# Kernel optimization log

Measured on AMD Instinct MI355X. Metric: run time of the kernel, lower is better.

## Reference

```python
import jax, jax.numpy as jnp
import numpy as np

NUM_EXPERTS = 8
TOP_K = 2


def setup_inputs() -> dict:
    key = jax.random.key(0)
    ks = jax.random.split(key, 8)
    B, S, D, H, E = 4, 2048, 1024, 2048, NUM_EXPERTS
    sd = 1.0 / np.sqrt(D)
    sh = 1.0 / np.sqrt(H)
    return {
        "x": jax.random.normal(ks[0], (B, S, D), dtype=jnp.float32),
        "noise": jax.random.normal(ks[1], (B, S, E), dtype=jnp.float32),
        "router_w": jax.random.normal(ks[2], (E, D), dtype=jnp.float32) * sd,
        "router_b": jnp.zeros((E,), dtype=jnp.float32),
        "noise_w": jax.random.normal(ks[3], (E, D), dtype=jnp.float32) * sd,
        "noise_b": jnp.zeros((E,), dtype=jnp.float32),
        "w1": jax.random.normal(ks[4], (E, H, D), dtype=jnp.float32) * sd,
        "w2": jax.random.normal(ks[5], (E, D, H), dtype=jnp.float32) * sh,
        "w3": jax.random.normal(ks[6], (E, H, D), dtype=jnp.float32) * sd,
    }


def reference(x, noise, router_w, router_b, noise_w, noise_b, w1, w2, w3):
    B, S, D = x.shape
    T = B * S
    xf = x.reshape(T, D)                                  # [T, D]
    noise_f = noise.reshape(T, -1)                        # [T, E]

    # Noisy top-k router
    logits = xf @ router_w.T + router_b                   # [T, E]
    noise_logits = xf @ noise_w.T + noise_b               # [T, E]
    noisy = logits + noise_f * jax.nn.softplus(noise_logits)
    top_vals, top_idx = jax.lax.top_k(noisy, TOP_K)       # [T, K]
    sparse = jnp.full_like(noisy, -jnp.inf)
    sparse = sparse.at[jnp.arange(T)[:, None], top_idx].set(top_vals)
    gates = jax.nn.softmax(sparse, axis=-1)               # [T, E]; zero off top-k

    # Expert SwiGLU combine. Gates are exactly 0 for non-selected experts, so
    # the masked gather/scatter loop of the original equals this weighted sum.
    out = jnp.zeros_like(xf)
    for i in range(NUM_EXPERTS):
        h = jax.nn.silu(xf @ w1[i].T) * (xf @ w3[i].T)    # [T, H]
        out = out + gates[:, i:i + 1] * (h @ w2[i].T)     # [T, D]
    return out.reshape(B, S, D)
```

## Files before the change

### kernel.cpp

```cpp
#include <hip/hip_runtime.h>

typedef unsigned short u16;
typedef __attribute__((ext_vector_type(8))) __bf16 bf16x8;
typedef __attribute__((ext_vector_type(8))) short short8;
typedef __attribute__((ext_vector_type(4))) float f32x4;

#define NE 8

#define SBAR()      asm volatile("s_barrier" ::: "memory")
#define WAIT_LGKM0() do { asm volatile("s_waitcnt lgkmcnt(0)" ::: "memory"); \
                          __builtin_amdgcn_sched_barrier(0); } while (0)
#define WAIT_VM4()  asm volatile("s_waitcnt vmcnt(4)" ::: "memory")
#define WAIT_VM0()  asm volatile("s_waitcnt vmcnt(0)" ::: "memory")

__device__ __forceinline__ u16 f2bf(float f) {
    union { float f; unsigned u; } v; v.f = f;
    unsigned u = v.u;
    return (u16)((u + 0x7fffu + ((u >> 16) & 1u)) >> 16);
}

__device__ __forceinline__ f32x4 mfma16(short8 a, short8 b, f32x4 c) {
    return __builtin_amdgcn_mfma_f32_16x16x32_bf16(
        __builtin_bit_cast(bf16x8, a), __builtin_bit_cast(bf16x8, b), c, 0, 0, 0);
}

__device__ __forceinline__ void gl2lds(const u16* g, u16* l) {
    __builtin_amdgcn_global_load_lds((const __attribute__((address_space(1))) void*)g,
                                     (__attribute__((address_space(3))) void*)l,
                                     16, 0, 0);
}

__global__ void cvt_kernel(const float* __restrict__ in, u16* __restrict__ out, size_t n4) {
    size_t i = (size_t)blockIdx.x * blockDim.x + threadIdx.x;
    size_t stride = (size_t)gridDim.x * blockDim.x;
    for (; i < n4; i += stride) {
        float4 v = ((const float4*)in)[i];
        ushort4 o;
        o.x = f2bf(v.x); o.y = f2bf(v.y); o.z = f2bf(v.z); o.w = f2bf(v.w);
        ((ushort4*)out)[i] = o;
    }
}

__global__ void cvt_w13_kernel(const float* __restrict__ w1, const float* __restrict__ w3,
                               u16* __restrict__ wc, int H, int D) {
    size_t n = (size_t)NE * H * (D / 4);
    size_t i = (size_t)blockIdx.x * blockDim.x + threadIdx.x;
    size_t stride = (size_t)gridDim.x * blockDim.x;
    int d4n = D / 4;
    for (; i < n; i += stride) {
        int d4 = (int)(i % d4n);
        size_t rem = i / d4n;
        int j = (int)(rem % H);
        int e = (int)(rem / H);
        float4 v1 = ((const float4*)w1)[i];
        float4 v3 = ((const float4*)w3)[i];
        ushort4 o1, o3;
        o1.x = f2bf(v1.x); o1.y = f2bf(v1.y); o1.z = f2bf(v1.z); o1.w = f2bf(v1.w);
        o3.x = f2bf(v3.x); o3.y = f2bf(v3.y); o3.z = f2bf(v3.z); o3.w = f2bf(v3.w);
        int wcrow = ((j >> 4) << 5) + (j & 15);
        size_t o = (((size_t)e * 2 * H + wcrow) * d4n + d4);
        ((ushort4*)wc)[o] = o1;
        ((ushort4*)wc)[o + (size_t)16 * d4n] = o3;
    }
}

__global__ void router_kernel(const float* __restrict__ x, const float* __restrict__ noise,
                              const float* __restrict__ rw, const float* __restrict__ rb,
                              const float* __restrict__ nw, const float* __restrict__ nb,
                              int* __restrict__ tops, float* __restrict__ gpair,
                              u16* __restrict__ xb, int T, int D) {
    int wv = threadIdx.x >> 6;
    int lane = threadIdx.x & 63;
    int t = blockIdx.x * 4 + wv;
    if (t >= T) return;

    const float4* x4 = (const float4*)(x + (size_t)t * D) + lane * 4;
    float4 xv0 = x4[0], xv1 = x4[1], xv2 = x4[2], xv3 = x4[3];

    {
        ushort4 s0, s1, s2, s3;
        s0.x = f2bf(xv0.x); s0.y = f2bf(xv0.y); s0.z = f2bf(xv0.z); s0.w = f2bf(xv0.w);
        s1.x = f2bf(xv1.x); s1.y = f2bf(xv1.y); s1.z = f2bf(xv1.z); s1.w = f2bf(xv1.w);
        s2.x = f2bf(xv2.x); s2.y = f2bf(xv2.y); s2.z = f2bf(xv2.z); s2.w = f2bf(xv2.w);
        s3.x = f2bf(xv3.x); s3.y = f2bf(xv3.y); s3.z = f2bf(xv3.z); s3.w = f2bf(xv3.w);
        ushort4* o = (ushort4*)(xb + (size_t)t * D + lane * 16);
        o[0] = s0; o[1] = s1; o[2] = s2; o[3] = s3;
    }

    float acc[2 * NE];
#pragma unroll
    for (int e = 0; e < NE; e++) {
        const float4* w4 = (const float4*)(rw + (size_t)e * D) + lane * 4;
        float4 a = w4[0], b = w4[1], c = w4[2], d = w4[3];
        acc[e] = xv0.x*a.x + xv0.y*a.y + xv0.z*a.z + xv0.w*a.w
               + xv1.x*b.x + xv1.y*b.y + xv1.z*b.z + xv1.w*b.w
               + xv2.x*c.x + xv2.y*c.y + xv2.z*c.z + xv2.w*c.w
               + xv3.x*d.x + xv3.y*d.y + xv3.z*d.z + xv3.w*d.w;
        const float4* v4 = (const float4*)(nw + (size_t)e * D) + lane * 4;
        a = v4[0]; b = v4[1]; c = v4[2]; d = v4[3];
        acc[NE + e] = xv0.x*a.x + xv0.y*a.y + xv0.z*a.z + xv0.w*a.w
                    + xv1.x*b.x + xv1.y*b.y + xv1.z*b.z + xv1.w*b.w
                    + xv2.x*c.x + xv2.y*c.y + xv2.z*c.z + xv2.w*c.w
                    + xv3.x*d.x + xv3.y*d.y + xv3.z*d.z + xv3.w*d.w;
    }
#pragma unroll
    for (int m = 1; m < 64; m <<= 1) {
#pragma unroll
        for (int k = 0; k < 2 * NE; k++) acc[k] += __shfl_xor(acc[k], m);
    }

    if (lane == 0) {
        float v0 = -1e30f, v1 = -1e30f;
        int i0 = 0, i1 = 0;
#pragma unroll
        for (int e = 0; e < NE; e++) {
            float z = acc[NE + e] + nb[e];
            float sp = (z > 20.f) ? z : log1pf(expf(z));
            float nv = acc[e] + rb[e] + noise[(size_t)t * NE + e] * sp;
            if (nv > v0) { v1 = v0; i1 = i0; v0 = nv; i0 = e; }
            else if (nv > v1) { v1 = nv; i1 = e; }
        }
        float e1 = expf(v1 - v0);
        float inv = 1.f / (1.f + e1);
        tops[t] = i0 | (i1 << 8);
        gpair[2 * t]     = inv;
        gpair[2 * t + 1] = e1 * inv;
    }
}

__global__ void build_kernel(const int* __restrict__ tops, const float* __restrict__ gpair,
                             int* __restrict__ counts, int* __restrict__ list,
                             float* __restrict__ glist, int* __restrict__ tokslot, int T) {
    int e = blockIdx.x;
    int tid = threadIdx.x, lane = tid & 63, wv = tid >> 6;
    __shared__ int wsum[4];
    __shared__ int sbase;
    if (tid == 0) sbase = 0;
    __syncthreads();
    for (int t0 = 0; t0 < T; t0 += 256) {
        int t = t0 + tid;
        int pk = tops[t];
        int i0 = pk & 0xff, i1 = (pk >> 8) & 0xff;
        bool f0 = (i0 == e), f1 = (i1 == e);
        bool f = f0 || f1;
        unsigned long long m = __ballot(f);
        int lpos = __popcll(m & (((unsigned long long)1 << lane) - 1ull));
        if (lane == 0) wsum[wv] = __popcll(m);
        __syncthreads();
        int woff = sbase;
        for (int w = 0; w < wv; w++) woff += wsum[w];
        int tot = wsum[0] + wsum[1] + wsum[2] + wsum[3];
        if (f) {
            int pos = woff + lpos;
            list[e * T + pos]  = t;
            glist[e * T + pos] = f0 ? gpair[2 * t] : gpair[2 * t + 1];
            tokslot[2 * t + (f0 ? 0 : 1)] = (e << 16) | pos;
        }
        __syncthreads();
        if (tid == 0) sbase += tot;
    }
    __syncthreads();
    if (tid == 0) counts[e] = sbase;
}

__global__ void scan_kernel(const int* __restrict__ counts, int* __restrict__ offsets,
                            int* __restrict__ bmap, int* __restrict__ nb) {
    if (threadIdx.x == 0 && blockIdx.x == 0) {
        int s = 0, t = 0;
        for (int e = 0; e < NE; e++) {
            offsets[e] = s;
            int c = counts[e];
            s += c;
            int m = (c + 255) >> 8;
            for (int i = 0; i < m; i++) bmap[t++] = (e << 16) | i;
        }
        offsets[NE] = s;
        nb[0] = t;
    }
}


#define FRAG_READS(abase, bbase, af, bf, mibase) do { \
        _Pragma("unroll") \
        for (int mi = 0; mi < 4; mi++) \
            af[mi] = *(const short8*)((abase) + aoff + ((mibase) + mi) * 512); \
        if (bf##_load) { \
            _Pragma("unroll") \
            for (int ni = 0; ni < 4; ni++) \
                bf[ni] = *(const short8*)((bbase) + boff + ni * 512); \
        } } while (0)

#define MFMA16X(af, bf, mibase) do { \
        __builtin_amdgcn_s_setprio(1); \
        _Pragma("unroll") \
        for (int mi = 0; mi < 4; mi++) \
            _Pragma("unroll") \
            for (int ni = 0; ni < 4; ni++) \
                acc[(mibase) + mi][ni] = mfma16(af[mi], bf[ni], acc[(mibase) + mi][ni]); \
        __builtin_amdgcn_s_setprio(0); } while (0)

__launch_bounds__(512, 2)
__global__ void gemm1_kernel(const u16* __restrict__ xb, const u16* __restrict__ wc,
                             const int* __restrict__ counts, const int* __restrict__ offsets,
                             const int* __restrict__ list, const float* __restrict__ glist,
                             const int* __restrict__ bmap, const int* __restrict__ nb,
                             u16* __restrict__ hb, int T, int D, int H) {
    if ((int)blockIdx.y >= nb[0]) return;
    int info = bmap[blockIdx.y];
    int e = info >> 16, mblk = info & 0xffff, nblk = blockIdx.x;
    int count = counts[e];

    __shared__ u16 sA[3 * 8192];
    __shared__ u16 sB[3 * 8192];
    __shared__ int stok[256];
    __shared__ float sgate[256];

    int tid = threadIdx.x;
    int lane = tid & 63, wid = tid >> 6;

    if (tid < 256) {
        int rr = min(mblk * 256 + tid, count - 1);
        stok[tid]  = list[e * T + rr];
        sgate[tid] = glist[e * T + rr];
    }
    __syncthreads();

    const u16* wcp = wc + ((size_t)e * 2 * H + nblk * 256) * D;

    int srow = tid >> 2, qs = tid & 3;
    int cchk = qs ^ ((srow >> 1) & 3);
    const u16* pa0 = xb + (size_t)stok[srow] * D + cchk * 8;
    const u16* pa1 = xb + (size_t)stok[128 + srow] * D + cchk * 8;
    const u16* pb0 = wcp + (size_t)srow * D + cchk * 8;
    const u16* pb1 = wcp + (size_t)(128 + srow) * D + cchk * 8;
    u16* dstA = sA + wid * 512;
    u16* dstB = sB + wid * 512;

    int r = lane & 15, q = lane >> 4;
    int cq = q ^ ((r >> 1) & 3);
    int wr = wid >> 2, wc4 = wid & 3;
    int aoff = (wr * 128 + r) * 32 + cq * 8;
    int boff = (wc4 * 64 + r) * 32 + cq * 8;

    f32x4 acc[8][4];
#pragma unroll
    for (int mi = 0; mi < 8; mi++)
#pragma unroll
        for (int ni = 0; ni < 4; ni++) acc[mi][ni] = (f32x4)0.f;

    gl2lds(pa0, dstA);          gl2lds(pb0, dstB);
    gl2lds(pa1, dstA + 4096);   gl2lds(pb1, dstB + 4096);
    pa0 += 32; pa1 += 32; pb0 += 32; pb1 += 32;
    gl2lds(pa0, dstA + 8192);          gl2lds(pb0, dstB + 8192);
    gl2lds(pa1, dstA + 8192 + 4096);   gl2lds(pb1, dstB + 8192 + 4096);
    pa0 += 32; pa1 += 32; pb0 += 32; pb1 += 32;
    WAIT_VM4();
    SBAR();

    const int nt = D >> 5;
    int cur = 0;
    for (int t = 0; t < nt; ++t) {
        const u16* abase = sA + cur * 8192;
        const u16* bbase = sB + cur * 8192;
        int stg = cur + 2; if (stg >= 3) stg -= 3;
        u16* asg = sA + stg * 8192 + wid * 512;
        u16* bsg = sB + stg * 8192 + wid * 512;
        bool st = (t + 2 < nt);

        short8 af[4], bf[4];
        const bool bf_load = true;
        FRAG_READS(abase, bbase, af, bf, 0);
        if (st) { gl2lds(pa0, asg); gl2lds(pb0, bsg); }
        SBAR();
        WAIT_LGKM0();
        MFMA16X(af, bf, 0);
        SBAR();
#pragma unroll
        for (int mi = 0; mi < 4; mi++)
            af[mi] = *(const short8*)(abase + aoff + (4 + mi) * 512);
        if (st) {
            gl2lds(pa1, asg + 4096); gl2lds(pb1, bsg + 4096);
            pa0 += 32; pa1 += 32; pb0 += 32; pb1 += 32;
        }
        SBAR();
        WAIT_LGKM0();
        MFMA16X(af, bf, 4);
        if (st) { WAIT_VM4(); } else { WAIT_VM0(); }
        SBAR();
        cur++; if (cur >= 3) cur = 0;
    }

    int hrow0 = offsets[e];
#pragma unroll
    for (int mi = 0; mi < 8; mi++) {
#pragma unroll
        for (int p = 0; p < 2; p++) {
            int col = nblk * 128 + wc4 * 32 + p * 16 + r;
#pragma unroll
            for (int tt = 0; tt < 4; tt++) {
                int lrow = wr * 128 + mi * 16 + q * 4 + tt;
                int grow = mblk * 256 + lrow;
                if (grow < count) {
                    float v = acc[mi][2 * p][tt];
                    float hv = v / (1.f + expf(-v)) * acc[mi][2 * p + 1][tt] * sgate[lrow];
                    hb[(size_t)(hrow0 + grow) * H + col] = f2bf(hv);
                }
            }
        }
    }
}

__launch_bounds__(512, 2)
__global__ void gemm2_kernel(const u16* __restrict__ hb, const u16* __restrict__ w2b,
                             const int* __restrict__ counts, const int* __restrict__ offsets,
                             const int* __restrict__ bmap, const int* __restrict__ nb,
                             float* __restrict__ o2, int T, int D, int H) {
    if ((int)blockIdx.y >= nb[0]) return;
    int info = bmap[blockIdx.y];
    int e = info >> 16, mblk = info & 0xffff, nblk = blockIdx.x;
    int count = counts[e];

    __shared__ u16 sA[3 * 8192];
    __shared__ u16 sB[3 * 8192];

    int tid = threadIdx.x;
    int lane = tid & 63, wid = tid >> 6;
    int off0 = offsets[e];
    const u16* w2p = w2b + ((size_t)e * D + nblk * 256) * H;

    int srow = tid >> 2, qs = tid & 3;
    int cchk = qs ^ ((srow >> 1) & 3);
    int ra0 = min(mblk * 256 + srow, count - 1);
    int ra1 = min(mblk * 256 + 128 + srow, count - 1);
    const u16* pa0 = hb + (size_t)(off0 + ra0) * H + cchk * 8;
    const u16* pa1 = hb + (size_t)(off0 + ra1) * H + cchk * 8;
    const u16* pb0 = w2p + (size_t)srow * H + cchk * 8;
    const u16* pb1 = w2p + (size_t)(128 + srow) * H + cchk * 8;
    u16* dstA = sA + wid * 512;
    u16* dstB = sB + wid * 512;

    int r = lane & 15, q = lane >> 4;
    int cq = q ^ ((r >> 1) & 3);
    int wr = wid >> 2, wc4 = wid & 3;
    int aoff = (wr * 128 + r) * 32 + cq * 8;
    int boff = (wc4 * 64 + r) * 32 + cq * 8;

    f32x4 acc[8][4];
#pragma unroll
    for (int mi = 0; mi < 8; mi++)
#pragma unroll
        for (int ni = 0; ni < 4; ni++) acc[mi][ni] = (f32x4)0.f;

    gl2lds(pa0, dstA);          gl2lds(pb0, dstB);
    gl2lds(pa1, dstA + 4096);   gl2lds(pb1, dstB + 4096);
    pa0 += 32; pa1 += 32; pb0 += 32; pb1 += 32;
    gl2lds(pa0, dstA + 8192);          gl2lds(pb0, dstB + 8192);
    gl2lds(pa1, dstA + 8192 + 4096);   gl2lds(pb1, dstB + 8192 + 4096);
    pa0 += 32; pa1 += 32; pb0 += 32; pb1 += 32;
    WAIT_VM4();
    SBAR();

    const int nt = H >> 5;
    int cur = 0;
    for (int t = 0; t < nt; ++t) {
        const u16* abase = sA + cur * 8192;
        const u16* bbase = sB + cur * 8192;
        int stg = cur + 2; if (stg >= 3) stg -= 3;
        u16* asg = sA + stg * 8192 + wid * 512;
        u16* bsg = sB + stg * 8192 + wid * 512;
        bool st = (t + 2 < nt);

        short8 af[4], bf[4];
        const bool bf_load = true;
        FRAG_READS(abase, bbase, af, bf, 0);
        if (st) { gl2lds(pa0, asg); gl2lds(pb0, bsg); }
        SBAR();
        WAIT_LGKM0();
        MFMA16X(af, bf, 0);
        SBAR();
#pragma unroll
        for (int mi = 0; mi < 4; mi++)
            af[mi] = *(const short8*)(abase + aoff + (4 + mi) * 512);
        if (st) {
            gl2lds(pa1, asg + 4096); gl2lds(pb1, bsg + 4096);
            pa0 += 32; pa1 += 32; pb0 += 32; pb1 += 32;
        }
        SBAR();
        WAIT_LGKM0();
        MFMA16X(af, bf, 4);
        if (st) { WAIT_VM4(); } else { WAIT_VM0(); }
        SBAR();
        cur++; if (cur >= 3) cur = 0;
    }

#pragma unroll
    for (int mi = 0; mi < 8; mi++) {
#pragma unroll
        for (int tt = 0; tt < 4; tt++) {
            int grow = mblk * 256 + wr * 128 + mi * 16 + q * 4 + tt;
            if (grow < count) {
#pragma unroll
                for (int ni = 0; ni < 4; ni++) {
                    int col = nblk * 256 + wc4 * 64 + ni * 16 + r;
                    o2[(size_t)(off0 + grow) * D + col] = acc[mi][ni][tt];
                }
            }
        }
    }
}

__global__ void combine_kernel(const float* __restrict__ o2, const int* __restrict__ tokslot,
                               const int* __restrict__ offsets, float* __restrict__ out, int D) {
    int t = blockIdx.x;
    int s0 = tokslot[2 * t], s1 = tokslot[2 * t + 1];
    size_t r0 = offsets[s0 >> 16] + (s0 & 0xffff);
    size_t r1 = offsets[s1 >> 16] + (s1 & 0xffff);
    int c = threadIdx.x * 4;
    float4 a = *(const float4*)(o2 + r0 * D + c);
    float4 b = *(const float4*)(o2 + r1 * D + c);
    float4 o; o.x = a.x + b.x; o.y = a.y + b.y; o.z = a.z + b.z; o.w = a.w + b.w;
    *(float4*)(out + (size_t)t * D + c) = o;
}

extern "C" void kernel_launch(void* const* d_in, const int* in_sizes, int n_in,
                              void* d_out, int out_size, void* d_ws, size_t ws_size,
                              hipStream_t stream) {
    const float* x     = (const float*)d_in[0];
    const float* noise = (const float*)d_in[1];
    const float* rw    = (const float*)d_in[2];
    const float* rb    = (const float*)d_in[3];
    const float* nw    = (const float*)d_in[4];
    const float* nb_   = (const float*)d_in[5];
    const float* w1    = (const float*)d_in[6];
    const float* w2    = (const float*)d_in[7];
    const float* w3    = (const float*)d_in[8];
    float* out = (float*)d_out;

    const int E = NE;
    const int D = in_sizes[2] / E;
    const int T = in_sizes[0] / D;
    const int H = in_sizes[6] / (E * D);

    auto al = [](size_t v) { return (v + 255) & ~(size_t)255; };
    char* p = (char*)d_ws;
    size_t o_counts  = 0;
    size_t o_offsets = 64;
    size_t o_nb      = 128;
    size_t o_bmap    = 256;
    size_t o_tslot   = al(o_bmap  + 2048);
    size_t o_list    = al(o_tslot + (size_t)2 * T * 4);
    size_t o_glist   = al(o_list  + (size_t)E * T * 4);
    size_t o_xb      = al(o_glist + (size_t)E * T * 4);
    size_t o_wc      = al(o_xb    + (size_t)T * D * 2);
    size_t o_w2b     = al(o_wc    + (size_t)E * 2 * H * D * 2);
    size_t o_hb      = al(o_w2b   + (size_t)E * D * H * 2);

    int*   counts  = (int*)(p + o_counts);
    int*   offsets = (int*)(p + o_offsets);
    int*   nblk    = (int*)(p + o_nb);
    int*   bmap    = (int*)(p + o_bmap);
    int*   tokslot = (int*)(p + o_tslot);
    int*   list    = (int*)(p + o_list);
    float* glist   = (float*)(p + o_glist);
    u16*   xb      = (u16*)(p + o_xb);
    u16*   wc      = (u16*)(p + o_wc);
    float* o2      = (float*)(p + o_wc);
    u16*   w2b     = (u16*)(p + o_w2b);
    u16*   hb      = (u16*)(p + o_hb);
    int*   tops    = (int*)(p + o_hb);
    float* gpair   = (float*)(p + o_hb + (size_t)T * 4);

    cvt_w13_kernel<<<2048, 256, 0, stream>>>(w1, w3, wc, H, D);
    cvt_kernel<<<2048, 256, 0, stream>>>(w2, w2b, (size_t)E * D * H / 4);

    router_kernel<<<(T + 3) / 4, 256, 0, stream>>>(x, noise, rw, rb, nw, nb_,
                                                   tops, gpair, xb, T, D);
    build_kernel<<<NE, 256, 0, stream>>>(tops, gpair, counts, list, glist, tokslot, T);
    scan_kernel<<<1, 64, 0, stream>>>(counts, offsets, bmap, nblk);

    int maxb = 2 * T / 256 + NE;
    dim3 g1(2 * H / 256, maxb, 1);
    gemm1_kernel<<<g1, 512, 0, stream>>>(xb, wc, counts, offsets, list, glist,
                                         bmap, nblk, hb, T, D, H);
    dim3 g2(D / 256, maxb, 1);
    gemm2_kernel<<<g2, 512, 0, stream>>>(hb, w2b, counts, offsets,
                                         bmap, nblk, o2, T, D, H);
    combine_kernel<<<T, 256, 0, stream>>>(o2, tokslot, offsets, out, D);
}
```

Baseline: 659.5 us.

## Restructure expert GEMMs to K=64 double-buffered tiles with four-phase pipeline

Both expert GEMM kernels move from a 3-stage ring of K=32 tiles to a double buffer of K=64 tiles. Each tile is consumed in four quadrant phases, interleaving partial A/B fragment reads and loads of the next tile with MFMA work. This halves the number of K iterations and the barriers per unit of work, and uses a new 8-way XOR swizzle for 128-byte rows. The output fragment-to-row/column mapping changes to match. Risks: more LDS per block (64KB), which may limit two blocks per CU, and more complex vmcnt accounting.

New measurement: 625.1 us. 5.2% less time.

```diff
diff --git a/kernel.cpp b/kernel.cpp
--- a/kernel.cpp
+++ b/kernel.cpp
@@ -10,8 +10,8 @@
 #define SBAR()      asm volatile("s_barrier" ::: "memory")
 #define WAIT_LGKM0() do { asm volatile("s_waitcnt lgkmcnt(0)" ::: "memory"); \
                           __builtin_amdgcn_sched_barrier(0); } while (0)
-#define WAIT_VM4()  asm volatile("s_waitcnt vmcnt(4)" ::: "memory")
-#define WAIT_VM0()  asm volatile("s_waitcnt vmcnt(0)" ::: "memory")
+#define WAIT_VM6()  asm volatile("s_waitcnt vmcnt(6)" ::: "memory")
+#define WAIT_VM8()  asm volatile("s_waitcnt vmcnt(8)" ::: "memory")
 
 __device__ __forceinline__ u16 f2bf(float f) {
     union { float f; unsigned u; } v; v.f = f;
@@ -180,24 +180,56 @@
 }
 
 
-#define FRAG_READS(abase, bbase, af, bf, mibase) do { \
-        _Pragma("unroll") \
-        for (int mi = 0; mi < 4; mi++) \
-            af[mi] = *(const short8*)((abase) + aoff + ((mibase) + mi) * 512); \
-        if (bf##_load) { \
-            _Pragma("unroll") \
-            for (int ni = 0; ni < 4; ni++) \
-                bf[ni] = *(const short8*)((bbase) + boff + ni * 512); \
-        } } while (0)
-
-#define MFMA16X(af, bf, mibase) do { \
-        __builtin_amdgcn_s_setprio(1); \
-        _Pragma("unroll") \
-        for (int mi = 0; mi < 4; mi++) \
-            _Pragma("unroll") \
-            for (int ni = 0; ni < 4; ni++) \
-                acc[(mibase) + mi][ni] = mfma16(af[mi], bf[ni], acc[(mibase) + mi][ni]); \
-        __builtin_amdgcn_s_setprio(0); } while (0)
+#define PH_RD_A(B, MQ) { \
+    _Pragma("unroll") for (int m4 = 0; m4 < 4; m4++) { \
+        aF[m4][0] = *(const short8*)&lds[B][0][(MQ)*8192 + aRow + m4*1024 + cA0]; \
+        aF[m4][1] = *(const short8*)&lds[B][0][(MQ)*8192 + aRow + m4*1024 + cA1]; } }
+
+#define PH_RD_B(B, NQ) { \
+    _Pragma("unroll") for (int n2 = 0; n2 < 2; n2++) { \
+        bF[n2][0] = *(const short8*)&lds[B][1][(NQ)*8192 + bRow + n2*1024 + cA0]; \
+        bF[n2][1] = *(const short8*)&lds[B][1][(NQ)*8192 + bRow + n2*1024 + cA1]; } }
+
+#define PH_MMA(MQ, NQ) do { \
+    __builtin_amdgcn_s_setprio(1); \
+    _Pragma("unroll") for (int m4 = 0; m4 < 4; m4++) \
+        _Pragma("unroll") for (int n2 = 0; n2 < 2; n2++) { \
+            acc[(MQ)*4+m4][(NQ)*2+n2] = mfma16(aF[m4][0], bF[n2][0], acc[(MQ)*4+m4][(NQ)*2+n2]); \
+            acc[(MQ)*4+m4][(NQ)*2+n2] = mfma16(aF[m4][1], bF[n2][1], acc[(MQ)*4+m4][(NQ)*2+n2]); } \
+    __builtin_amdgcn_s_setprio(0); } while (0)
+
+#define STAGE(B, AB, H, p0, p1) do { \
+    u16* d_ = &lds[B][AB][(H)*8192 + wid*512]; \
+    gl2lds(p0, d_); gl2lds(p1, d_ + 4096); \
+    p0 += 64; p1 += 64; } while (0)
+
+#define G_TILE(B, u, nt) do { \
+     \
+    PH_RD_A(B, 0); PH_RD_B(B, 0); \
+    if ((u) + 1 < (nt)) STAGE((B)^1, 0, 1, pA10, pA11); \
+    SBAR(); WAIT_LGKM0(); \
+    PH_MMA(0, 0); \
+    WAIT_VM6(); \
+    SBAR(); \
+     \
+    PH_RD_B(B, 1); \
+    if ((u) + 1 < (nt)) STAGE((B)^1, 1, 1, pB10, pB11); \
+    SBAR(); WAIT_LGKM0(); \
+    PH_MMA(0, 1); \
+    SBAR(); \
+     \
+    PH_RD_A(B, 1); PH_RD_B(B, 0); \
+    if ((u) + 2 < (nt)) STAGE(B, 0, 0, pA00, pA01); \
+    SBAR(); WAIT_LGKM0(); \
+    PH_MMA(1, 0); \
+    SBAR(); \
+     \
+    PH_RD_B(B, 1); \
+    if ((u) + 2 < (nt)) STAGE(B, 1, 0, pB00, pB01); \
+    SBAR(); WAIT_LGKM0(); \
+    PH_MMA(1, 1); \
+    WAIT_VM8(); \
+    SBAR(); } while (0)
 
 __launch_bounds__(512, 2)
 __global__ void gemm1_kernel(const u16* __restrict__ xb, const u16* __restrict__ wc,
@@ -210,8 +242,7 @@
     int e = info >> 16, mblk = info & 0xffff, nblk = blockIdx.x;
     int count = counts[e];
 
-    __shared__ u16 sA[3 * 8192];
-    __shared__ u16 sB[3 * 8192];
+    __shared__ u16 lds[2][2][16384];
     __shared__ int stok[256];
     __shared__ float sgate[256];
 
@@ -225,22 +256,26 @@
     }
     __syncthreads();
 
-    const u16* wcp = wc + ((size_t)e * 2 * H + nblk * 256) * D;
-
-    int srow = tid >> 2, qs = tid & 3;
-    int cchk = qs ^ ((srow >> 1) & 3);
-    const u16* pa0 = xb + (size_t)stok[srow] * D + cchk * 8;
-    const u16* pa1 = xb + (size_t)stok[128 + srow] * D + cchk * 8;
-    const u16* pb0 = wcp + (size_t)srow * D + cchk * 8;
-    const u16* pb1 = wcp + (size_t)(128 + srow) * D + cchk * 8;
-    u16* dstA = sA + wid * 512;
-    u16* dstB = sB + wid * 512;
+    const u16* wcp = wc + ((size_t)e * 2 * H + (size_t)nblk * 256) * D;
+
+    int row_local = tid >> 3, c8 = tid & 7;
+    int c_glob = c8 ^ (row_local & 7);
+    const u16* pA00 = xb + (size_t)stok[row_local] * D + c_glob * 8;
+    const u16* pA01 = xb + (size_t)stok[64 + row_local] * D + c_glob * 8;
+    const u16* pA10 = xb + (size_t)stok[128 + row_local] * D + c_glob * 8;
+    const u16* pA11 = xb + (size_t)stok[192 + row_local] * D + c_glob * 8;
+    const u16* pB00 = wcp + (size_t)row_local * D + c_glob * 8;
+    const u16* pB01 = wcp + (size_t)(64 + row_local) * D + c_glob * 8;
+    const u16* pB10 = wcp + (size_t)(128 + row_local) * D + c_glob * 8;
+    const u16* pB11 = wcp + (size_t)(192 + row_local) * D + c_glob * 8;
 
     int r = lane & 15, q = lane >> 4;
-    int cq = q ^ ((r >> 1) & 3);
+    int swz = r & 7;
+    int cA0 = (q ^ swz) * 8;
+    int cA1 = ((q + 4) ^ swz) * 8;
     int wr = wid >> 2, wc4 = wid & 3;
-    int aoff = (wr * 128 + r) * 32 + cq * 8;
-    int boff = (wc4 * 64 + r) * 32 + cq * 8;
+    int aRow = (wr * 64 + r) * 64;
+    int bRow = (wc4 * 32 + r) * 64;
 
     f32x4 acc[8][4];
 #pragma unroll
@@ -248,61 +283,37 @@
 #pragma unroll
         for (int ni = 0; ni < 4; ni++) acc[mi][ni] = (f32x4)0.f;
 
-    gl2lds(pa0, dstA);          gl2lds(pb0, dstB);
-    gl2lds(pa1, dstA + 4096);   gl2lds(pb1, dstB + 4096);
-    pa0 += 32; pa1 += 32; pb0 += 32; pb1 += 32;
-    gl2lds(pa0, dstA + 8192);          gl2lds(pb0, dstB + 8192);
-    gl2lds(pa1, dstA + 8192 + 4096);   gl2lds(pb1, dstB + 8192 + 4096);
-    pa0 += 32; pa1 += 32; pb0 += 32; pb1 += 32;
-    WAIT_VM4();
+    short8 aF[4][2], bF[2][2];
+
+    STAGE(0, 0, 0, pA00, pA01);
+    STAGE(0, 0, 1, pA10, pA11);
+    STAGE(0, 1, 0, pB00, pB01);
+    STAGE(0, 1, 1, pB10, pB11);
+    STAGE(1, 0, 0, pA00, pA01);
+    STAGE(1, 1, 0, pB00, pB01);
+    WAIT_VM6();
     SBAR();
 
-    const int nt = D >> 5;
-    int cur = 0;
-    for (int t = 0; t < nt; ++t) {
-        const u16* abase = sA + cur * 8192;
-        const u16* bbase = sB + cur * 8192;
-        int stg = cur + 2; if (stg >= 3) stg -= 3;
-        u16* asg = sA + stg * 8192 + wid * 512;
-        u16* bsg = sB + stg * 8192 + wid * 512;
-        bool st = (t + 2 < nt);
-
-        short8 af[4], bf[4];
-        const bool bf_load = true;
-        FRAG_READS(abase, bbase, af, bf, 0);
-        if (st) { gl2lds(pa0, asg); gl2lds(pb0, bsg); }
-        SBAR();
-        WAIT_LGKM0();
-        MFMA16X(af, bf, 0);
-        SBAR();
-#pragma unroll
-        for (int mi = 0; mi < 4; mi++)
-            af[mi] = *(const short8*)(abase + aoff + (4 + mi) * 512);
-        if (st) {
-            gl2lds(pa1, asg + 4096); gl2lds(pb1, bsg + 4096);
-            pa0 += 32; pa1 += 32; pb0 += 32; pb1 += 32;
-        }
-        SBAR();
-        WAIT_LGKM0();
-        MFMA16X(af, bf, 4);
-        if (st) { WAIT_VM4(); } else { WAIT_VM0(); }
-        SBAR();
-        cur++; if (cur >= 3) cur = 0;
+    const int nt = D >> 6;
+    for (int u = 0; u < nt; u += 2) {
+        G_TILE(0, u, nt);
+        G_TILE(1, u + 1, nt);
     }
 
     int hrow0 = offsets[e];
 #pragma unroll
     for (int mi = 0; mi < 8; mi++) {
-#pragma unroll
-        for (int p = 0; p < 2; p++) {
-            int col = nblk * 128 + wc4 * 32 + p * 16 + r;
+        int lrow0 = (mi >> 2) * 128 + wr * 64 + (mi & 3) * 16 + q * 4;
+#pragma unroll
+        for (int a = 0; a < 2; a++) {
+            int col = nblk * 128 + a * 64 + wc4 * 16 + r;
 #pragma unroll
             for (int tt = 0; tt < 4; tt++) {
-                int lrow = wr * 128 + mi * 16 + q * 4 + tt;
+                int lrow = lrow0 + tt;
                 int grow = mblk * 256 + lrow;
                 if (grow < count) {
-                    float v = acc[mi][2 * p][tt];
-                    float hv = v / (1.f + expf(-v)) * acc[mi][2 * p + 1][tt] * sgate[lrow];
+                    float v = acc[mi][2 * a][tt];
+                    float hv = v / (1.f + expf(-v)) * acc[mi][2 * a + 1][tt] * sgate[lrow];
                     hb[(size_t)(hrow0 + grow) * H + col] = f2bf(hv);
                 }
             }
@@ -320,30 +331,35 @@
     int e = info >> 16, mblk = info & 0xffff, nblk = blockIdx.x;
     int count = counts[e];
 
-    __shared__ u16 sA[3 * 8192];
-    __shared__ u16 sB[3 * 8192];
+    __shared__ u16 lds[2][2][16384];
 
     int tid = threadIdx.x;
     int lane = tid & 63, wid = tid >> 6;
     int off0 = offsets[e];
-    const u16* w2p = w2b + ((size_t)e * D + nblk * 256) * H;
-
-    int srow = tid >> 2, qs = tid & 3;
-    int cchk = qs ^ ((srow >> 1) & 3);
-    int ra0 = min(mblk * 256 + srow, count - 1);
-    int ra1 = min(mblk * 256 + 128 + srow, count - 1);
-    const u16* pa0 = hb + (size_t)(off0 + ra0) * H + cchk * 8;
-    const u16* pa1 = hb + (size_t)(off0 + ra1) * H + cchk * 8;
-    const u16* pb0 = w2p + (size_t)srow * H + cchk * 8;
-    const u16* pb1 = w2p + (size_t)(128 + srow) * H + cchk * 8;
-    u16* dstA = sA + wid * 512;
-    u16* dstB = sB + wid * 512;
+    const u16* w2p = w2b + ((size_t)e * D + (size_t)nblk * 256) * H;
+
+    int row_local = tid >> 3, c8 = tid & 7;
+    int c_glob = c8 ^ (row_local & 7);
+    int ra00 = min(mblk * 256 + row_local, count - 1);
+    int ra01 = min(mblk * 256 + 64 + row_local, count - 1);
+    int ra10 = min(mblk * 256 + 128 + row_local, count - 1);
+    int ra11 = min(mblk * 256 + 192 + row_local, count - 1);
+    const u16* pA00 = hb + (size_t)(off0 + ra00) * H + c_glob * 8;
+    const u16* pA01 = hb + (size_t)(off0 + ra01) * H + c_glob * 8;
+    const u16* pA10 = hb + (size_t)(off0 + ra10) * H + c_glob * 8;
+    const u16* pA11 = hb + (size_t)(off0 + ra11) * H + c_glob * 8;
+    const u16* pB00 = w2p + (size_t)row_local * H + c_glob * 8;
+    const u16* pB01 = w2p + (size_t)(64 + row_local) * H + c_glob * 8;
+    const u16* pB10 = w2p + (size_t)(128 + row_local) * H + c_glob * 8;
+    const u16* pB11 = w2p + (size_t)(192 + row_local) * H + c_glob * 8;
 
     int r = lane & 15, q = lane >> 4;
-    int cq = q ^ ((r >> 1) & 3);
+    int swz = r & 7;
+    int cA0 = (q ^ swz) * 8;
+    int cA1 = ((q + 4) ^ swz) * 8;
     int wr = wid >> 2, wc4 = wid & 3;
-    int aoff = (wr * 128 + r) * 32 + cq * 8;
-    int boff = (wc4 * 64 + r) * 32 + cq * 8;
+    int aRow = (wr * 64 + r) * 64;
+    int bRow = (wc4 * 32 + r) * 64;
 
     f32x4 acc[8][4];
 #pragma unroll
@@ -351,57 +367,33 @@
 #pragma unroll
         for (int ni = 0; ni < 4; ni++) acc[mi][ni] = (f32x4)0.f;
 
-    gl2lds(pa0, dstA);          gl2lds(pb0, dstB);
-    gl2lds(pa1, dstA + 4096);   gl2lds(pb1, dstB + 4096);
-    pa0 += 32; pa1 += 32; pb0 += 32; pb1 += 32;
-    gl2lds(pa0, dstA + 8192);          gl2lds(pb0, dstB + 8192);
-    gl2lds(pa1, dstA + 8192 + 4096);   gl2lds(pb1, dstB + 8192 + 4096);
-    pa0 += 32; pa1 += 32; pb0 += 32; pb1 += 32;
-    WAIT_VM4();
+    short8 aF[4][2], bF[2][2];
+
+    STAGE(0, 0, 0, pA00, pA01);
+    STAGE(0, 0, 1, pA10, pA11);
+    STAGE(0, 1, 0, pB00, pB01);
+    STAGE(0, 1, 1, pB10, pB11);
+    STAGE(1, 0, 0, pA00, pA01);
+    STAGE(1, 1, 0, pB00, pB01);
+    WAIT_VM6();
     SBAR();
 
-    const int nt = H >> 5;
-    int cur = 0;
-    for (int t = 0; t < nt; ++t) {
-        const u16* abase = sA + cur * 8192;
-        const u16* bbase = sB + cur * 8192;
-        int stg = cur + 2; if (stg >= 3) stg -= 3;
-        u16* asg = sA + stg * 8192 + wid * 512;
-        u16* bsg = sB + stg * 8192 + wid * 512;
-        bool st = (t + 2 < nt);
-
-        short8 af[4], bf[4];
-        const bool bf_load = true;
-        FRAG_READS(abase, bbase, af, bf, 0);
-        if (st) { gl2lds(pa0, asg); gl2lds(pb0, bsg); }
-        SBAR();
-        WAIT_LGKM0();
-        MFMA16X(af, bf, 0);
-        SBAR();
-#pragma unroll
-        for (int mi = 0; mi < 4; mi++)
-            af[mi] = *(const short8*)(abase + aoff + (4 + mi) * 512);
-        if (st) {
-            gl2lds(pa1, asg + 4096); gl2lds(pb1, bsg + 4096);
-            pa0 += 32; pa1 += 32; pb0 += 32; pb1 += 32;
-        }
-        SBAR();
-        WAIT_LGKM0();
-        MFMA16X(af, bf, 4);
-        if (st) { WAIT_VM4(); } else { WAIT_VM0(); }
-        SBAR();
-        cur++; if (cur >= 3) cur = 0;
+    const int nt = H >> 6;
+    for (int u = 0; u < nt; u += 2) {
+        G_TILE(0, u, nt);
+        G_TILE(1, u + 1, nt);
     }
 
 #pragma unroll
     for (int mi = 0; mi < 8; mi++) {
+        int lrow0 = (mi >> 2) * 128 + wr * 64 + (mi & 3) * 16 + q * 4;
 #pragma unroll
         for (int tt = 0; tt < 4; tt++) {
-            int grow = mblk * 256 + wr * 128 + mi * 16 + q * 4 + tt;
+            int grow = mblk * 256 + lrow0 + tt;
             if (grow < count) {
 #pragma unroll
                 for (int ni = 0; ni < 4; ni++) {
-                    int col = nblk * 256 + wc4 * 64 + ni * 16 + r;
+                    int col = nblk * 256 + (ni >> 1) * 128 + wc4 * 32 + (ni & 1) * 16 + r;
                     o2[(size_t)(off0 + grow) * D + col] = acc[mi][ni][tt];
                 }
             }
```
